# Performance work log

Measured on AMD Instinct MI355X. Metric: run time of the kernel, lower is better.

## Reference

```python
import jax, jax.numpy as jnp
import numpy as np

DIM = 256
NUM_HEADS = 4
HEAD_DIM = DIM // NUM_HEADS


def setup_inputs() -> dict:
    key = jax.random.key(0)
    ks = jax.random.split(key, 8)
    B, N, C = 4, 2048, DIM
    x = jax.random.normal(ks[0], (B, N, C), dtype=jnp.float32)
    R = jax.random.normal(ks[1], (B, 3, 3), dtype=jnp.float32)
    P = jax.random.normal(ks[2], (N, 3), dtype=jnp.float32)
    s = 1.0 / np.sqrt(C)
    qkv_w = jax.random.normal(ks[3], (3 * C, C), dtype=jnp.float32) * s
    qkv_b = jax.random.normal(ks[4], (3 * C,), dtype=jnp.float32) * 0.02
    proj_w = jax.random.normal(ks[5], (C, C), dtype=jnp.float32) * s
    proj_b = jax.random.normal(ks[6], (C,), dtype=jnp.float32) * 0.02
    pos_scale = jnp.asarray(1.0, dtype=jnp.float32)
    return {"x": x, "R": R, "P": P, "qkv_w": qkv_w, "qkv_b": qkv_b,
            "proj_w": proj_w, "proj_b": proj_b, "pos_scale": pos_scale}


def reference(x, R, P, qkv_w, qkv_b, proj_w, proj_b, pos_scale):
    B, N, C = x.shape
    H, D = NUM_HEADS, HEAD_DIM
    scale = D ** -0.5
    # qkv: (B,N,3C) -> (3,B,H,N,D)
    qkv = (x @ qkv_w.T + qkv_b).reshape(B, N, 3, H, D).transpose(2, 0, 3, 1, 4)
    q, k, v = qkv[0], qkv[1], qkv[2]
    # attention logits (B,H,N,N)
    attn = jnp.einsum('bhid,bhjd->bhij', q, k) * scale
    # positional bias: RP = (R @ P^T)^T -> (B,N,3); bias_ij = dot(RP_i, P_j)
    RP = jnp.einsum('bab,jb->bja', R, P) if False else jnp.einsum('bca,ja->bjc', jnp.swapaxes(R, 1, 2), P)
    RP = jnp.einsum('bcd,jd->bjc', R, P)  # (B,N,3): (R @ P.T).T
    bias = jnp.einsum('bik,jk->bij', RP, P)[:, None, :, :] * pos_scale  # (B,1,N,N) broadcast over heads
    attn = jax.nn.softmax(attn + bias, axis=-1)
    out = jnp.einsum('bhij,bhjd->bhid', attn, v)  # (B,H,N,D)
    out = out.transpose(0, 2, 1, 3).reshape(B, N, C)
    out = out @ proj_w.T + proj_b
    return out
```

## Files before the change

### kernel.cpp

```cpp
#include <hip/hip_runtime.h>
#include <hip/hip_bf16.h>

#define B_ 4
#define N_ 2048
#define C_ 256
#define H_ 4
#define D_ 64

typedef __attribute__((ext_vector_type(8))) short bf16x8;
typedef __attribute__((ext_vector_type(4))) float f32x4;

#define LOG2E 1.4426950408889634f

static __device__ inline unsigned short f2bf(float f) {
    unsigned u = __builtin_bit_cast(unsigned, f);
    unsigned r = (u + 0x7fffu + ((u >> 16) & 1u)) >> 16;
    return (unsigned short)r;
}
static __device__ inline float bf2f(unsigned short h) {
    unsigned u = ((unsigned)h) << 16;
    return __builtin_bit_cast(float, u);
}
static __device__ inline unsigned pack2(float a, float b) {
    __hip_bfloat162 h = __float22bfloat162_rn(make_float2(a, b));
    unsigned u;
    __builtin_memcpy(&u, &h, 4);
    return u;
}
static __device__ inline bf16x8 ld_frag(const unsigned short* p) {
    return __builtin_bit_cast(bf16x8, *(const uint4*)p);
}

__global__ __launch_bounds__(256) void cvt_kernel(
    const float* __restrict__ x, const float* __restrict__ qkv_w,
    const float* __restrict__ proj_w, const float* __restrict__ Pm,
    unsigned short* __restrict__ xb, unsigned short* __restrict__ wqb,
    unsigned short* __restrict__ wpb, unsigned* __restrict__ nb)
{
    __shared__ float red[256];
    const int bid = blockIdx.x, tid = threadIdx.x;
    const float* s; unsigned short* d; int i;
    if (bid < 1024)      { s = x;      d = xb;  i = (bid * 256 + tid) * 8; }
    else if (bid < 1120) { s = qkv_w;  d = wqb; i = ((bid - 1024) * 256 + tid) * 8; }
    else                 { s = proj_w; d = wpb; i = ((bid - 1120) * 256 + tid) * 8; }
    float4 a = *(const float4*)(s + i);
    float4 b = *(const float4*)(s + i + 4);
    uint4 u;
    u.x = pack2(a.x, a.y); u.y = pack2(a.z, a.w);
    u.z = pack2(b.x, b.y); u.w = pack2(b.z, b.w);
    *(uint4*)(d + i) = u;

    if (bid == 1151) {
        float mp = 0.f;
        #pragma unroll
        for (int r = 0; r < 8; ++r) {
            int n = tid * 8 + r;
            float p0 = Pm[n * 3 + 0], p1 = Pm[n * 3 + 1], p2 = Pm[n * 3 + 2];
            mp = fmaxf(mp, p0 * p0 + p1 * p1 + p2 * p2);
        }
        red[tid] = mp;
        __syncthreads();
        for (int w = 128; w > 0; w >>= 1) {
            if (tid < w) red[tid] = fmaxf(red[tid], red[tid + w]);
            __syncthreads();
        }
        if (tid < 16) nb[tid] = 0u;
        if (tid == 0) nb[16] = __builtin_bit_cast(unsigned, red[0]);
    }
}

__global__ __launch_bounds__(256) void qkv_gemm(
    const unsigned short* __restrict__ xb, const unsigned short* __restrict__ wb,
    const float* __restrict__ bias, unsigned short* __restrict__ qb,
    unsigned short* __restrict__ kb, unsigned short* __restrict__ vt)
{
    __shared__ __align__(16) unsigned short As[128 * 40];
    __shared__ __align__(16) unsigned short Bs[128 * 40];
    const int m0 = blockIdx.x * 128, o0 = blockIdx.y * 128;
    const int tid = threadIdx.x;
    const int wave = tid >> 6, lane = tid & 63, quad = lane >> 4, l16 = lane & 15;
    const int wy = wave >> 1, wx = wave & 1;

    f32x4 acc[4][4];
    #pragma unroll
    for (int i = 0; i < 4; ++i)
        #pragma unroll
        for (int j = 0; j < 4; ++j) acc[i][j] = (f32x4){0.f, 0.f, 0.f, 0.f};

    const int srow = tid >> 1, soff = (tid & 1) * 16;

    for (int k0 = 0; k0 < 256; k0 += 32) {
        __syncthreads();
        {
            const unsigned short* sa = &xb[(size_t)(m0 + srow) * 256 + k0 + soff];
            const unsigned short* sb = &wb[(size_t)(o0 + srow) * 256 + k0 + soff];
            *(uint4*)&As[srow * 40 + soff + 0] = *(const uint4*)(sa + 0);
            *(uint4*)&As[srow * 40 + soff + 8] = *(const uint4*)(sa + 8);
            *(uint4*)&Bs[srow * 40 + soff + 0] = *(const uint4*)(sb + 0);
            *(uint4*)&Bs[srow * 40 + soff + 8] = *(const uint4*)(sb + 8);
        }
        __syncthreads();
        bf16x8 a[4], b[4];
        #pragma unroll
        for (int mt = 0; mt < 4; ++mt) a[mt] = ld_frag(&As[(wy * 64 + mt * 16 + l16) * 40 + quad * 8]);
        #pragma unroll
        for (int nt = 0; nt < 4; ++nt) b[nt] = ld_frag(&Bs[(wx * 64 + nt * 16 + l16) * 40 + quad * 8]);
        #pragma unroll
        for (int mt = 0; mt < 4; ++mt)
            #pragma unroll
            for (int nt = 0; nt < 4; ++nt)
                acc[mt][nt] = __builtin_amdgcn_mfma_f32_16x16x32_bf16(a[mt], b[nt], acc[mt][nt], 0, 0, 0);
    }

    const int sec = o0 + wx * 64;
    const int three = sec >> 8;
    const int h = (sec >> 6) & 3;
    const int b = m0 >> 11;
    float bv[4];
    #pragma unroll
    for (int nt = 0; nt < 4; ++nt) bv[nt] = bias[sec + nt * 16 + l16];

    if (three == 2) {
        const int n64 = (m0 + wy * 64) & 2047;
        const size_t bh64 = ((size_t)b * H_ + h) * 64;
        #pragma unroll
        for (int nt = 0; nt < 4; ++nt) {
            int d = nt * 16 + l16;
            #pragma unroll
            for (int r = 0; r < 4; ++r) {
                ushort4 v;
                v.x = f2bf(acc[0][nt][r] + bv[nt]);
                v.y = f2bf(acc[1][nt][r] + bv[nt]);
                v.z = f2bf(acc[2][nt][r] + bv[nt]);
                v.w = f2bf(acc[3][nt][r] + bv[nt]);
                *(ushort4*)&vt[(bh64 + d) * N_ + n64 + 16 * quad + 4 * r] = v;
            }
        }
    } else {
        unsigned short* dst = (three == 0) ? qb : kb;
        float sc = (three == 0) ? (0.125f * LOG2E) : 1.0f;
        #pragma unroll
        for (int mt = 0; mt < 4; ++mt)
            #pragma unroll
            for (int r = 0; r < 4; ++r) {
                int n = (m0 + wy * 64 + mt * 16 + quad * 4 + r) & 2047;
                size_t rowbase = (((size_t)b * H_ + h) * N_ + n) * D_;
                #pragma unroll
                for (int nt = 0; nt < 4; ++nt)
                    dst[rowbase + nt * 16 + l16] = f2bf((acc[mt][nt][r] + bv[nt]) * sc);
            }
    }
}

__global__ __launch_bounds__(256) void norm_kernel(
    const unsigned short* __restrict__ kb, unsigned* __restrict__ nb)
{
    __shared__ float red[256];
    const int bh = blockIdx.x, chunk = blockIdx.y, tid = threadIdx.x;
    const size_t base = (size_t)bh * N_ * D_ + (size_t)(chunk * 256 + tid) * D_;
    float sk = 0.f;
    #pragma unroll
    for (int j4 = 0; j4 < 8; ++j4) {
        union { uint4 u; unsigned short s[8]; } kv;
        kv.u = *(const uint4*)&kb[base + j4 * 8];
        #pragma unroll
        for (int j = 0; j < 8; ++j) { float v = bf2f(kv.s[j]); sk += v * v; }
    }
    red[tid] = sk;
    __syncthreads();
    for (int w = 128; w > 0; w >>= 1) {
        if (tid < w) red[tid] = fmaxf(red[tid], red[tid + w]);
        __syncthreads();
    }
    if (tid == 0) atomicMax(&nb[bh], __builtin_bit_cast(unsigned, red[0]));
}

#define LDK 72
#define LDKX 104

__global__ __launch_bounds__(256) void attn_kernel(
    const unsigned short* __restrict__ qb, const unsigned short* __restrict__ kb,
    const unsigned short* __restrict__ vt,
    const float* __restrict__ Rm, const float* __restrict__ Pm,
    const float* __restrict__ ps_ptr, const unsigned* __restrict__ nb,
    unsigned short* __restrict__ Opart, float* __restrict__ ml)
{
    __shared__ __align__(16) unsigned short Ks[64 * LDKX];
    __shared__ __align__(16) unsigned short Vs[64 * LDK];
    __shared__ __align__(16) unsigned short Ps[64 * LDK];

    const int bh = blockIdx.y;
    const int b = bh >> 2;
    const int i0 = blockIdx.x * 64;
    const int split = blockIdx.z;
    const int tid = threadIdx.x;
    const int wave = tid >> 6, lane = tid & 63;
    const int quad = lane >> 4, l16 = lane & 15;
    const float ps = ps_ptr[0];

    const size_t base = (size_t)bh * N_ * D_;
    const unsigned short* qg = qb + base;
    const unsigned short* kg = kb + base;
    const unsigned short* vg = vt + base;

    if (tid < 64) {
        uint4 z = {0u, 0u, 0u, 0u};
        *(uint4*)&Ks[tid * LDKX + 80] = z;
        *(uint4*)&Ks[tid * LDKX + 88] = z;
    }

    const int qrow = i0 + wave * 16 + l16;
    bf16x8 aq[3];
    #pragma unroll
    for (int ks = 0; ks < 2; ++ks)
        aq[ks] = ld_frag(&qg[(size_t)qrow * D_ + ks * 32 + quad * 8]);

    float rpn;
    {
        float p0 = Pm[qrow * 3 + 0], p1 = Pm[qrow * 3 + 1], p2 = Pm[qrow * 3 + 2];
        float sc = ps * LOG2E;
        unsigned short ah[3], al[3];
        float s2 = 0.f;
        #pragma unroll
        for (int c = 0; c < 3; ++c) {
            float a = (Rm[b * 9 + c * 3 + 0] * p0 + Rm[b * 9 + c * 3 + 1] * p1
                     + Rm[b * 9 + c * 3 + 2] * p2) * sc;
            s2 += a * a;
            ah[c] = f2bf(a);
            al[c] = f2bf(a - bf2f(ah[c]));
        }
        rpn = s2;
        bf16x8 e = (bf16x8){0,0,0,0,0,0,0,0};
        if (quad == 0) {
            e[0] = (short)ah[0]; e[1] = (short)ah[1]; e[2] = (short)ah[2];
            e[3] = (short)ah[0]; e[4] = (short)ah[1]; e[5] = (short)ah[2];
            e[6] = (short)al[0]; e[7] = (short)al[1];
        } else if (quad == 1) {
            e[0] = (short)al[2];
        }
        aq[2] = e;
    }

    float Mrow[4];
    {
        float qn = 0.f;
        #pragma unroll
        for (int ks = 0; ks < 2; ++ks)
            #pragma unroll
            for (int j = 0; j < 8; ++j) {
                float v = bf2f((unsigned short)aq[ks][j]);
                qn += v * v;
            }
        qn += __shfl_xor(qn, 16);
        qn += __shfl_xor(qn, 32);
        const float maxK = sqrtf(__builtin_bit_cast(float, nb[bh]));
        const float maxP = sqrtf(__builtin_bit_cast(float, nb[16]));
        #pragma unroll
        for (int r = 0; r < 4; ++r) {
            float qrn = sqrtf(__shfl(qn, quad * 4 + r));
            float arn = sqrtf(__shfl(rpn, quad * 4 + r));
            Mrow[r] = qrn * maxK + arn * maxP + 1.0f;
        }
    }

    const bf16x8 ones = (bf16x8){0x3F80,0x3F80,0x3F80,0x3F80,0x3F80,0x3F80,0x3F80,0x3F80};

    f32x4 o_acc[4], lacc;
    #pragma unroll
    for (int t = 0; t < 4; ++t) o_acc[t] = (f32x4){0.f, 0.f, 0.f, 0.f};
    lacc = (f32x4){0.f, 0.f, 0.f, 0.f};

    const int jbeg = split * (N_ / 2);
    const int NT = (N_ / 2) / 64;

    for (int jt = 0; jt < NT; ++jt) {
        const int j0 = jbeg + jt * 64;
        __syncthreads();
        #pragma unroll
        for (int rr = 0; rr < 2; ++rr) {
            int c = tid + rr * 256;
            int row = c >> 3, off = (c & 7) * 8;
            *(uint4*)&Ks[row * LDKX + off] = *(const uint4*)&kg[(size_t)(j0 + row) * D_ + off];
            *(uint4*)&Vs[row * LDK + off] = *(const uint4*)&vg[(size_t)row * N_ + j0 + off];
        }
        if (tid < 64) {
            const float* pp = &Pm[(size_t)(j0 + tid) * 3];
            float p0 = pp[0], p1 = pp[1], p2 = pp[2];
            unsigned u0 = f2bf(p0), u1 = f2bf(p1), u2 = f2bf(p2);
            unsigned v0 = f2bf(p0 - bf2f((unsigned short)u0));
            unsigned v1 = f2bf(p1 - bf2f((unsigned short)u1));
            unsigned v2 = f2bf(p2 - bf2f((unsigned short)u2));
            uint4 lo, hi;
            lo.x = u0 | (u1 << 16); lo.y = u2 | (v0 << 16);
            lo.z = v1 | (v2 << 16); lo.w = u0 | (u1 << 16);
            hi.x = u2; hi.y = 0u; hi.z = 0u; hi.w = 0u;
            *(uint4*)&Ks[tid * LDKX + 64] = lo;
            *(uint4*)&Ks[tid * LDKX + 72] = hi;
        }
        __syncthreads();

        f32x4 s[4];
        #pragma unroll
        for (int t = 0; t < 4; ++t) {
            f32x4 c = {0.f, 0.f, 0.f, 0.f};
            #pragma unroll
            for (int ks = 0; ks < 3; ++ks) {
                bf16x8 bk = ld_frag(&Ks[(l16 + 16 * t) * LDKX + ks * 32 + quad * 8]);
                c = __builtin_amdgcn_mfma_f32_16x16x32_bf16(aq[ks], bk, c, 0, 0, 0);
            }
            s[t] = c;
        }

        #pragma unroll
        for (int r = 0; r < 4; ++r) {
            float p0 = exp2f(s[0][r] - Mrow[r]), p1 = exp2f(s[1][r] - Mrow[r]);
            float p2 = exp2f(s[2][r] - Mrow[r]), p3 = exp2f(s[3][r] - Mrow[r]);
            uint2 w;
            w.x = pack2(p0, p1);
            w.y = pack2(p2, p3);
            *(uint2*)&Ps[(wave * 16 + quad * 4 + r) * LDK + 4 * l16] = w;
        }

        #pragma unroll
        for (int ks = 0; ks < 2; ++ks) {
            bf16x8 ap = ld_frag(&Ps[(wave * 16 + l16) * LDK + ks * 32 + quad * 8]);
            #pragma unroll
            for (int t = 0; t < 4; ++t) {
                bf16x8 bv = ld_frag(&Vs[(l16 + 16 * t) * LDK + ks * 32 + quad * 8]);
                o_acc[t] = __builtin_amdgcn_mfma_f32_16x16x32_bf16(ap, bv, o_acc[t], 0, 0, 0);
            }
            lacc = __builtin_amdgcn_mfma_f32_16x16x32_bf16(ap, ones, lacc, 0, 0, 0);
        }
    }

    const size_t pbase = (size_t)(split * 16 + bh) * N_;
    #pragma unroll
    for (int r = 0; r < 4; ++r) {
        int row = i0 + wave * 16 + quad * 4 + r;
        #pragma unroll
        for (int t = 0; t < 4; ++t)
            Opart[(pbase + row) * D_ + l16 + 16 * t] = f2bf(o_acc[t][r]);
        if (l16 == 0)
            ml[pbase + row] = lacc[r];
    }
}

__global__ __launch_bounds__(256) void proj_gemm(
    const unsigned short* __restrict__ Opart, const float* __restrict__ ml,
    const unsigned short* __restrict__ wb, const float* __restrict__ bias,
    float* __restrict__ out)
{
    __shared__ __align__(16) unsigned short As[64 * 40];
    __shared__ __align__(16) unsigned short Bs[64 * 40];
    const int m0 = blockIdx.x * 64, o0 = blockIdx.y * 64;
    const int tid = threadIdx.x;
    const int wave = tid >> 6, lane = tid & 63, quad = lane >> 4, l16 = lane & 15;

    const int srow = tid >> 2, scb = (tid & 3) * 8;
    const int sm = m0 + srow, sb = sm >> 11, sn = sm & 2047;

    float invh[4];
    #pragma unroll
    for (int h = 0; h < 4; ++h) {
        size_t r1 = (size_t)(sb * 4 + h) * N_ + sn;
        invh[h] = 1.f / (ml[r1] + ml[r1 + 16 * (size_t)N_]);
    }

    f32x4 acc[4];
    #pragma unroll
    for (int j = 0; j < 4; ++j) acc[j] = (f32x4){0.f, 0.f, 0.f, 0.f};

    for (int k0 = 0; k0 < 256; k0 += 32) {
        const int h = k0 >> 6;
        const int d0 = (k0 & 63) + scb;
        __syncthreads();
        {
            size_t r1 = (size_t)(sb * 4 + h) * N_ + sn;
            union { uint4 u; unsigned short s[8]; } a1, a2;
            a1.u = *(const uint4*)&Opart[r1 * D_ + d0];
            a2.u = *(const uint4*)&Opart[(r1 + 16 * (size_t)N_) * D_ + d0];
            float w = invh[h];
            uint4 mv;
            unsigned* mp = (unsigned*)&mv;
            #pragma unroll
            for (int j = 0; j < 4; ++j)
                mp[j] = pack2((bf2f(a1.s[2*j]) + bf2f(a2.s[2*j])) * w,
                              (bf2f(a1.s[2*j+1]) + bf2f(a2.s[2*j+1])) * w);
            *(uint4*)&As[srow * 40 + scb] = mv;
            *(uint4*)&Bs[srow * 40 + scb] = *(const uint4*)&wb[(size_t)(o0 + srow) * 256 + k0 + scb];
        }
        __syncthreads();
        bf16x8 a = ld_frag(&As[(wave * 16 + l16) * 40 + quad * 8]);
        #pragma unroll
        for (int nt = 0; nt < 4; ++nt) {
            bf16x8 b = ld_frag(&Bs[(nt * 16 + l16) * 40 + quad * 8]);
            acc[nt] = __builtin_amdgcn_mfma_f32_16x16x32_bf16(a, b, acc[nt], 0, 0, 0);
        }
    }

    float bv[4];
    #pragma unroll
    for (int nt = 0; nt < 4; ++nt) bv[nt] = bias[o0 + nt * 16 + l16];
    #pragma unroll
    for (int r = 0; r < 4; ++r) {
        int m = m0 + wave * 16 + quad * 4 + r;
        #pragma unroll
        for (int nt = 0; nt < 4; ++nt)
            out[(size_t)m * 256 + o0 + nt * 16 + l16] = acc[nt][r] + bv[nt];
    }
}

extern "C" void kernel_launch(void* const* d_in, const int* in_sizes, int n_in,
                              void* d_out, int out_size, void* d_ws, size_t ws_size,
                              hipStream_t stream) {
    const float* x       = (const float*)d_in[0];
    const float* Rm      = (const float*)d_in[1];
    const float* Pm      = (const float*)d_in[2];
    const float* qkv_w   = (const float*)d_in[3];
    const float* qkv_b   = (const float*)d_in[4];
    const float* proj_w  = (const float*)d_in[5];
    const float* proj_b  = (const float*)d_in[6];
    const float* pos_scl = (const float*)d_in[7];
    float* out = (float*)d_out;

    const size_t NE = (size_t)B_ * H_ * N_ * D_;
    unsigned short* xb    = (unsigned short*)d_ws;
    unsigned short* wqb   = xb   + NE;
    unsigned short* wpb   = wqb  + 768 * 256;
    unsigned short* qb    = wpb  + 256 * 256;
    unsigned short* kb    = qb   + NE;
    unsigned short* vtb   = kb   + NE;
    unsigned short* opart = vtb  + NE;
    float*          mlb   = (float*)(opart + 2 * NE);
    unsigned*       nb    = (unsigned*)(mlb + 2 * 16 * 2048);

    cvt_kernel<<<1152, 256, 0, stream>>>(x, qkv_w, proj_w, Pm, xb, wqb, wpb, nb);
    qkv_gemm<<<dim3(64, 6), 256, 0, stream>>>(xb, wqb, qkv_b, qb, kb, vtb);
    norm_kernel<<<dim3(16, 8), 256, 0, stream>>>(kb, nb);
    attn_kernel<<<dim3(32, 16, 2), 256, 0, stream>>>(qb, kb, vtb, Rm, Pm, pos_scl, nb, opart, mlb);
    proj_gemm<<<dim3(128, 4), 256, 0, stream>>>(opart, mlb, wpb, proj_b, out);
}
```

Measured before the change: 147.3 us.

## Compute transposed attention with K/V fragments loaded directly from global memory

The attention kernel is restructured to compute S^T with keys as the MFMA A operand: K, the precomputed position-extension fragments, and V^T fragments are loaded straight from global into registers per wave. Q, the bias extension and the per-row softmax bound are kept in shared memory once per block. The per-tile K/V shared-memory staging and one of the two barriers are removed, and the P tile is double-buffered. The position bf16 hi/lo split moves into the conversion kernel, and the V^T and output store layouts change to match. The risk is that direct global fragment loads without prefetch expose memory latency each iteration.

```diff
diff --git a/kernel.cpp b/kernel.cpp
--- a/kernel.cpp
+++ b/kernel.cpp
@@ -27,6 +27,9 @@
     __builtin_memcpy(&u, &h, 4);
     return u;
 }
+static __device__ inline unsigned pks(unsigned short a, unsigned short b) {
+    return (unsigned)a | ((unsigned)b << 16);
+}
 static __device__ inline bf16x8 ld_frag(const unsigned short* p) {
     return __builtin_bit_cast(bf16x8, *(const uint4*)p);
 }
@@ -35,7 +38,8 @@
     const float* __restrict__ x, const float* __restrict__ qkv_w,
     const float* __restrict__ proj_w, const float* __restrict__ Pm,
     unsigned short* __restrict__ xb, unsigned short* __restrict__ wqb,
-    unsigned short* __restrict__ wpb, unsigned* __restrict__ nb)
+    unsigned short* __restrict__ wpb, unsigned short* __restrict__ pext,
+    unsigned* __restrict__ nb)
 {
     __shared__ float red[256];
     const int bid = blockIdx.x, tid = threadIdx.x;
@@ -52,11 +56,23 @@
 
     if (bid == 1151) {
         float mp = 0.f;
-        #pragma unroll
-        for (int r = 0; r < 8; ++r) {
-            int n = tid * 8 + r;
+        for (int r8 = 0; r8 < 8; ++r8) {
+            int n = tid * 8 + r8;
             float p0 = Pm[n * 3 + 0], p1 = Pm[n * 3 + 1], p2 = Pm[n * 3 + 2];
             mp = fmaxf(mp, p0 * p0 + p1 * p1 + p2 * p2);
+            unsigned short u0 = f2bf(p0), u1 = f2bf(p1), u2 = f2bf(p2);
+            unsigned short v0 = f2bf(p0 - bf2f(u0));
+            unsigned short v1 = f2bf(p1 - bf2f(u1));
+            unsigned short v2 = f2bf(p2 - bf2f(u2));
+            uint4 q0, q1, z = {0u, 0u, 0u, 0u};
+            q0.x = pks(u0, u1); q0.y = pks(u2, u0);
+            q0.z = pks(u1, u2); q0.w = pks(v0, v1);
+            q1.x = pks(v2, 0); q1.y = 0u; q1.z = 0u; q1.w = 0u;
+            unsigned short* pr = &pext[(size_t)n * 32];
+            *(uint4*)(pr + 0) = q0;
+            *(uint4*)(pr + 8) = q1;
+            *(uint4*)(pr + 16) = z;
+            *(uint4*)(pr + 24) = z;
         }
         red[tid] = mp;
         __syncthreads();
@@ -125,15 +141,15 @@
         const size_t bh64 = ((size_t)b * H_ + h) * 64;
         #pragma unroll
         for (int nt = 0; nt < 4; ++nt) {
-            int d = nt * 16 + l16;
-            #pragma unroll
-            for (int r = 0; r < 4; ++r) {
+            int dd = nt * 16 + l16;
+            #pragma unroll
+            for (int mt = 0; mt < 4; ++mt) {
                 ushort4 v;
-                v.x = f2bf(acc[0][nt][r] + bv[nt]);
-                v.y = f2bf(acc[1][nt][r] + bv[nt]);
-                v.z = f2bf(acc[2][nt][r] + bv[nt]);
-                v.w = f2bf(acc[3][nt][r] + bv[nt]);
-                *(ushort4*)&vt[(bh64 + d) * N_ + n64 + 16 * quad + 4 * r] = v;
+                v.x = f2bf(acc[mt][nt][0] + bv[nt]);
+                v.y = f2bf(acc[mt][nt][1] + bv[nt]);
+                v.z = f2bf(acc[mt][nt][2] + bv[nt]);
+                v.w = f2bf(acc[mt][nt][3] + bv[nt]);
+                *(ushort4*)&vt[(bh64 + dd) * N_ + n64 + mt * 16 + quad * 4] = v;
             }
         }
     } else {
@@ -175,22 +191,21 @@
     if (tid == 0) atomicMax(&nb[bh], __builtin_bit_cast(unsigned, red[0]));
 }
 
-#define LDK 72
-#define LDKX 104
+#define QLD 104
+#define PLD 72
 
 __global__ __launch_bounds__(256) void attn_kernel(
     const unsigned short* __restrict__ qb, const unsigned short* __restrict__ kb,
-    const unsigned short* __restrict__ vt,
+    const unsigned short* __restrict__ vt, const unsigned short* __restrict__ pext,
     const float* __restrict__ Rm, const float* __restrict__ Pm,
     const float* __restrict__ ps_ptr, const unsigned* __restrict__ nb,
     unsigned short* __restrict__ Opart, float* __restrict__ ml)
 {
-    __shared__ __align__(16) unsigned short Ks[64 * LDKX];
-    __shared__ __align__(16) unsigned short Vs[64 * LDK];
-    __shared__ __align__(16) unsigned short Ps[64 * LDK];
-
-    const int bh = blockIdx.y;
-    const int b = bh >> 2;
+    __shared__ __align__(16) unsigned short Qs[64 * QLD];
+    __shared__ __align__(16) unsigned short Pb[2][64 * PLD];
+    __shared__ float MqS[64];
+
+    const int bh = blockIdx.y, b = bh >> 2;
     const int i0 = blockIdx.x * 64;
     const int split = blockIdx.z;
     const int tid = threadIdx.x;
@@ -203,65 +218,52 @@
     const unsigned short* kg = kb + base;
     const unsigned short* vg = vt + base;
 
+    {
+        int row = tid >> 2, c = (tid & 3) * 16;
+        const unsigned short* src = &qg[(size_t)(i0 + row) * D_ + c];
+        *(uint4*)&Qs[row * QLD + c + 0] = *(const uint4*)(src + 0);
+        *(uint4*)&Qs[row * QLD + c + 8] = *(const uint4*)(src + 8);
+    }
     if (tid < 64) {
-        uint4 z = {0u, 0u, 0u, 0u};
-        *(uint4*)&Ks[tid * LDKX + 80] = z;
-        *(uint4*)&Ks[tid * LDKX + 88] = z;
-    }
-
-    const int qrow = i0 + wave * 16 + l16;
-    bf16x8 aq[3];
-    #pragma unroll
-    for (int ks = 0; ks < 2; ++ks)
-        aq[ks] = ld_frag(&qg[(size_t)qrow * D_ + ks * 32 + quad * 8]);
-
-    float rpn;
-    {
-        float p0 = Pm[qrow * 3 + 0], p1 = Pm[qrow * 3 + 1], p2 = Pm[qrow * 3 + 2];
+        const int q = i0 + tid;
+        float p0 = Pm[q * 3 + 0], p1 = Pm[q * 3 + 1], p2 = Pm[q * 3 + 2];
         float sc = ps * LOG2E;
         unsigned short ah[3], al[3];
-        float s2 = 0.f;
+        float an2 = 0.f;
         #pragma unroll
         for (int c = 0; c < 3; ++c) {
             float a = (Rm[b * 9 + c * 3 + 0] * p0 + Rm[b * 9 + c * 3 + 1] * p1
                      + Rm[b * 9 + c * 3 + 2] * p2) * sc;
-            s2 += a * a;
+            an2 += a * a;
             ah[c] = f2bf(a);
             al[c] = f2bf(a - bf2f(ah[c]));
         }
-        rpn = s2;
-        bf16x8 e = (bf16x8){0,0,0,0,0,0,0,0};
-        if (quad == 0) {
-            e[0] = (short)ah[0]; e[1] = (short)ah[1]; e[2] = (short)ah[2];
-            e[3] = (short)ah[0]; e[4] = (short)ah[1]; e[5] = (short)ah[2];
-            e[6] = (short)al[0]; e[7] = (short)al[1];
-        } else if (quad == 1) {
-            e[0] = (short)al[2];
-        }
-        aq[2] = e;
-    }
+        uint4 e0, e1, z = {0u, 0u, 0u, 0u};
+        e0.x = pks(ah[0], ah[1]); e0.y = pks(ah[2], al[0]);
+        e0.z = pks(al[1], al[2]); e0.w = pks(ah[0], ah[1]);
+        e1.x = pks(ah[2], 0); e1.y = 0u; e1.z = 0u; e1.w = 0u;
+        unsigned short* er = &Qs[tid * QLD + 64];
+        *(uint4*)(er + 0) = e0;
+        *(uint4*)(er + 8) = e1;
+        *(uint4*)(er + 16) = z;
+        *(uint4*)(er + 24) = z;
+        float qn = 0.f;
+        #pragma unroll
+        for (int c8 = 0; c8 < 8; ++c8) {
+            union { uint4 u; unsigned short s[8]; } qv;
+            qv.u = *(const uint4*)&qg[(size_t)q * D_ + c8 * 8];
+            #pragma unroll
+            for (int j = 0; j < 8; ++j) { float v = bf2f(qv.s[j]); qn += v * v; }
+        }
+        float maxK = sqrtf(__builtin_bit_cast(float, nb[bh]));
+        float maxP = sqrtf(__builtin_bit_cast(float, nb[16]));
+        MqS[tid] = sqrtf(qn) * maxK + sqrtf(an2) * maxP + 1.0f;
+    }
+    __syncthreads();
 
     float Mrow[4];
-    {
-        float qn = 0.f;
-        #pragma unroll
-        for (int ks = 0; ks < 2; ++ks)
-            #pragma unroll
-            for (int j = 0; j < 8; ++j) {
-                float v = bf2f((unsigned short)aq[ks][j]);
-                qn += v * v;
-            }
-        qn += __shfl_xor(qn, 16);
-        qn += __shfl_xor(qn, 32);
-        const float maxK = sqrtf(__builtin_bit_cast(float, nb[bh]));
-        const float maxP = sqrtf(__builtin_bit_cast(float, nb[16]));
-        #pragma unroll
-        for (int r = 0; r < 4; ++r) {
-            float qrn = sqrtf(__shfl(qn, quad * 4 + r));
-            float arn = sqrtf(__shfl(rpn, quad * 4 + r));
-            Mrow[r] = qrn * maxK + arn * maxP + 1.0f;
-        }
-    }
+    #pragma unroll
+    for (int t = 0; t < 4; ++t) Mrow[t] = MqS[16 * t + l16];
 
     const bf16x8 ones = (bf16x8){0x3F80,0x3F80,0x3F80,0x3F80,0x3F80,0x3F80,0x3F80,0x3F80};
 
@@ -272,77 +274,62 @@
 
     const int jbeg = split * (N_ / 2);
     const int NT = (N_ / 2) / 64;
-
+    const int wkey = wave * 16 + l16;
+    const int vrow = wave * 16 + l16;
+
+    int buf = 0;
     for (int jt = 0; jt < NT; ++jt) {
         const int j0 = jbeg + jt * 64;
-        __syncthreads();
-        #pragma unroll
-        for (int rr = 0; rr < 2; ++rr) {
-            int c = tid + rr * 256;
-            int row = c >> 3, off = (c & 7) * 8;
-            *(uint4*)&Ks[row * LDKX + off] = *(const uint4*)&kg[(size_t)(j0 + row) * D_ + off];
-            *(uint4*)&Vs[row * LDK + off] = *(const uint4*)&vg[(size_t)row * N_ + j0 + off];
-        }
-        if (tid < 64) {
-            const float* pp = &Pm[(size_t)(j0 + tid) * 3];
-            float p0 = pp[0], p1 = pp[1], p2 = pp[2];
-            unsigned u0 = f2bf(p0), u1 = f2bf(p1), u2 = f2bf(p2);
-            unsigned v0 = f2bf(p0 - bf2f((unsigned short)u0));
-            unsigned v1 = f2bf(p1 - bf2f((unsigned short)u1));
-            unsigned v2 = f2bf(p2 - bf2f((unsigned short)u2));
-            uint4 lo, hi;
-            lo.x = u0 | (u1 << 16); lo.y = u2 | (v0 << 16);
-            lo.z = v1 | (v2 << 16); lo.w = u0 | (u1 << 16);
-            hi.x = u2; hi.y = 0u; hi.z = 0u; hi.w = 0u;
-            *(uint4*)&Ks[tid * LDKX + 64] = lo;
-            *(uint4*)&Ks[tid * LDKX + 72] = hi;
-        }
-        __syncthreads();
+        bf16x8 ka0 = ld_frag(&kg[(size_t)(j0 + wkey) * D_ + quad * 8]);
+        bf16x8 ka1 = ld_frag(&kg[(size_t)(j0 + wkey) * D_ + 32 + quad * 8]);
+        bf16x8 kae = ld_frag(&pext[(size_t)(j0 + wkey) * 32 + quad * 8]);
+        bf16x8 va0 = ld_frag(&vg[(size_t)vrow * N_ + j0 + quad * 8]);
+        bf16x8 va1 = ld_frag(&vg[(size_t)vrow * N_ + j0 + 32 + quad * 8]);
 
         f32x4 s[4];
         #pragma unroll
         for (int t = 0; t < 4; ++t) {
+            const unsigned short* br = &Qs[(16 * t + l16) * QLD];
             f32x4 c = {0.f, 0.f, 0.f, 0.f};
-            #pragma unroll
-            for (int ks = 0; ks < 3; ++ks) {
-                bf16x8 bk = ld_frag(&Ks[(l16 + 16 * t) * LDKX + ks * 32 + quad * 8]);
-                c = __builtin_amdgcn_mfma_f32_16x16x32_bf16(aq[ks], bk, c, 0, 0, 0);
+            c = __builtin_amdgcn_mfma_f32_16x16x32_bf16(ka0, ld_frag(br + quad * 8), c, 0, 0, 0);
+            c = __builtin_amdgcn_mfma_f32_16x16x32_bf16(ka1, ld_frag(br + 32 + quad * 8), c, 0, 0, 0);
+            c = __builtin_amdgcn_mfma_f32_16x16x32_bf16(kae, ld_frag(br + 64 + quad * 8), c, 0, 0, 0);
+            s[t] = c;
+        }
+
+        #pragma unroll
+        for (int t = 0; t < 4; ++t) {
+            uint2 w;
+            w.x = pack2(exp2f(s[t][0] - Mrow[t]), exp2f(s[t][1] - Mrow[t]));
+            w.y = pack2(exp2f(s[t][2] - Mrow[t]), exp2f(s[t][3] - Mrow[t]));
+            *(uint2*)&Pb[buf][(16 * t + l16) * PLD + wave * 16 + quad * 4] = w;
+        }
+        __syncthreads();
+
+        #pragma unroll
+        for (int ks = 0; ks < 2; ++ks) {
+            bf16x8 av = ks ? va1 : va0;
+            #pragma unroll
+            for (int t = 0; t < 4; ++t) {
+                bf16x8 bp = ld_frag(&Pb[buf][(16 * t + l16) * PLD + ks * 32 + quad * 8]);
+                o_acc[t] = __builtin_amdgcn_mfma_f32_16x16x32_bf16(av, bp, o_acc[t], 0, 0, 0);
             }
-            s[t] = c;
-        }
-
-        #pragma unroll
-        for (int r = 0; r < 4; ++r) {
-            float p0 = exp2f(s[0][r] - Mrow[r]), p1 = exp2f(s[1][r] - Mrow[r]);
-            float p2 = exp2f(s[2][r] - Mrow[r]), p3 = exp2f(s[3][r] - Mrow[r]);
-            uint2 w;
-            w.x = pack2(p0, p1);
-            w.y = pack2(p2, p3);
-            *(uint2*)&Ps[(wave * 16 + quad * 4 + r) * LDK + 4 * l16] = w;
-        }
-
-        #pragma unroll
-        for (int ks = 0; ks < 2; ++ks) {
-            bf16x8 ap = ld_frag(&Ps[(wave * 16 + l16) * LDK + ks * 32 + quad * 8]);
-            #pragma unroll
-            for (int t = 0; t < 4; ++t) {
-                bf16x8 bv = ld_frag(&Vs[(l16 + 16 * t) * LDK + ks * 32 + quad * 8]);
-                o_acc[t] = __builtin_amdgcn_mfma_f32_16x16x32_bf16(ap, bv, o_acc[t], 0, 0, 0);
-            }
-            lacc = __builtin_amdgcn_mfma_f32_16x16x32_bf16(ap, ones, lacc, 0, 0, 0);
-        }
+            bf16x8 bl = ld_frag(&Pb[buf][(16 * wave + l16) * PLD + ks * 32 + quad * 8]);
+            lacc = __builtin_amdgcn_mfma_f32_16x16x32_bf16(ones, bl, lacc, 0, 0, 0);
+        }
+        buf ^= 1;
     }
 
     const size_t pbase = (size_t)(split * 16 + bh) * N_;
     #pragma unroll
-    for (int r = 0; r < 4; ++r) {
-        int row = i0 + wave * 16 + quad * 4 + r;
-        #pragma unroll
-        for (int t = 0; t < 4; ++t)
-            Opart[(pbase + row) * D_ + l16 + 16 * t] = f2bf(o_acc[t][r]);
-        if (l16 == 0)
-            ml[pbase + row] = lacc[r];
-    }
+    for (int t = 0; t < 4; ++t) {
+        ushort4 v;
+        v.x = f2bf(o_acc[t][0]); v.y = f2bf(o_acc[t][1]);
+        v.z = f2bf(o_acc[t][2]); v.w = f2bf(o_acc[t][3]);
+        *(ushort4*)&Opart[(pbase + i0 + 16 * t + l16) * D_ + wave * 16 + quad * 4] = v;
+    }
+    if (quad == 0)
+        ml[pbase + i0 + wave * 16 + l16] = lacc[0];
 }
 
 __global__ __launch_bounds__(256) void proj_gemm(
@@ -427,16 +414,17 @@
     unsigned short* xb    = (unsigned short*)d_ws;
     unsigned short* wqb   = xb   + NE;
     unsigned short* wpb   = wqb  + 768 * 256;
-    unsigned short* qb    = wpb  + 256 * 256;
+    unsigned short* pextb = wpb  + 256 * 256;
+    unsigned short* qb    = pextb + 2048 * 32;
     unsigned short* kb    = qb   + NE;
     unsigned short* vtb   = kb   + NE;
     unsigned short* opart = vtb  + NE;
     float*          mlb   = (float*)(opart + 2 * NE);
     unsigned*       nb    = (unsigned*)(mlb + 2 * 16 * 2048);
 
-    cvt_kernel<<<1152, 256, 0, stream>>>(x, qkv_w, proj_w, Pm, xb, wqb, wpb, nb);
+    cvt_kernel<<<1152, 256, 0, stream>>>(x, qkv_w, proj_w, Pm, xb, wqb, wpb, pextb, nb);
     qkv_gemm<<<dim3(64, 6), 256, 0, stream>>>(xb, wqb, qkv_b, qb, kb, vtb);
     norm_kernel<<<dim3(16, 8), 256, 0, stream>>>(kb, nb);
-    attn_kernel<<<dim3(32, 16, 2), 256, 0, stream>>>(qb, kb, vtb, Rm, Pm, pos_scl, nb, opart, mlb);
+    attn_kernel<<<dim3(32, 16, 2), 256, 0, stream>>>(qb, kb, vtb, pextb, Rm, Pm, pos_scl, nb, opart, mlb);
     proj_gemm<<<dim3(128, 4), 256, 0, stream>>>(opart, mlb, wpb, proj_b, out);
 }
```

Measured after the change: 147.4 us. Within noise of the previous version (+0.1%).
